# Optimization experiments

Hardware: AMD Instinct MI355X
Metric: run time of the kernel (lower is better)

Reference implementation:

```python
import jax, jax.numpy as jnp
import numpy as np

N_NODES = 50000
N_EDGES = 800000
N_FEAT = 128
HIDDEN = 16
N_CLASSES = 16


def spline_conv(x, src, dst, u, weight, root, bias, num_nodes):
    """SplineConv, dim=1, kernel_size=2, degree=1, open spline, aggr='mean'.

    x: [N, in], weight: [2, in, out], u: [E, 1] pseudo-coords in [0, 1).
    Linear B-spline basis over 2 knots: basis = (1-u, u) -> W[0], W[1].
    Transform at node level first (cheaper than per-edge when E > N),
    then gather along edges and scatter-mean to targets.
    """
    h = jnp.einsum('ni,kio->kno', x, weight)  # [2, N, out]
    msg = (1.0 - u) * h[0][src] + u * h[1][src]  # [E, out]
    agg = jax.ops.segment_sum(msg, dst, num_segments=num_nodes)
    deg = jax.ops.segment_sum(jnp.ones((src.shape[0],), x.dtype), dst,
                              num_segments=num_nodes)
    agg = agg / jnp.maximum(deg, 1.0)[:, None]
    return agg + x @ root + bias


def setup_inputs() -> dict:
    key = jax.random.key(0)
    ks = jax.random.split(key, 8)
    x = jax.random.normal(ks[0], (N_NODES, N_FEAT), dtype=jnp.float32)
    edge_index = jax.random.randint(ks[1], (2, N_EDGES), 0, N_NODES, dtype=jnp.int32)
    edge_attr = jax.random.uniform(ks[2], (N_EDGES, 1), dtype=jnp.float32)
    s1 = 1.0 / np.sqrt(N_FEAT)
    s2 = 1.0 / np.sqrt(HIDDEN)
    return {
        'x': x,
        'edge_index': edge_index,
        'edge_attr': edge_attr,
        'w1': jax.random.normal(ks[3], (2, N_FEAT, HIDDEN), dtype=jnp.float32) * s1,
        'root1': jax.random.normal(ks[4], (N_FEAT, HIDDEN), dtype=jnp.float32) * s1,
        'b1': jnp.zeros((HIDDEN,), dtype=jnp.float32),
        'w2': jax.random.normal(ks[5], (2, HIDDEN, N_CLASSES), dtype=jnp.float32) * s2,
        'root2': jax.random.normal(ks[6], (HIDDEN, N_CLASSES), dtype=jnp.float32) * s2,
        'b2': jnp.zeros((N_CLASSES,), dtype=jnp.float32),
    }


def reference(x, edge_index, edge_attr, w1, root1, b1, w2, root2, b2):
    src, dst = edge_index[0], edge_index[1]
    n = x.shape[0]
    # eval mode: F.dropout(training=False) is identity
    h = jax.nn.elu(spline_conv(x, src, dst, edge_attr, w1, root1, b1, n))
    out = spline_conv(h, src, dst, edge_attr, w2, root2, b2, n)
    return jax.nn.log_softmax(out, axis=1)
```

## Files before the change

### kernel.cpp

```cpp
#include <hip/hip_runtime.h>
#include <hip/hip_bf16.h>
#include <math.h>

#define N_NODES 50000
#define N_EDGES 800000
#define N_FEAT 128
#define HIDDEN 16
#define N_CLASSES 16

#define NBUCK 782
#define PB_NB 196
#define PB_E  4096
#define BCAP  1600

typedef __attribute__((ext_vector_type(8))) short short8v;
typedef __attribute__((ext_vector_type(4))) float floatx4;

__device__ __forceinline__ float bf2f(unsigned int bits16) {
    return __uint_as_float(bits16 << 16);
}
__device__ __forceinline__ unsigned int f2bf_bits(float f) {
    __hip_bfloat16 h = __float2bfloat16(f);
    return (unsigned int)*reinterpret_cast<unsigned short*>(&h);
}

__global__ __launch_bounds__(256) void k_node1(
    const float* __restrict__ x, const float* __restrict__ w1,
    const float* __restrict__ root1, const float* __restrict__ b1,
    unsigned int* __restrict__ ABu, float* __restrict__ C)
{
    int lane = threadIdx.x & 63;
    int wid  = threadIdx.x >> 6;
    int m = lane & 15;
    int q = lane >> 4;
    int nb = blockIdx.x * 64 + wid * 16;

    short8v bf[3][4];
#pragma unroll
    for (int c = 0; c < 4; ++c) {
        int k0 = c * 32 + q * 8;
        const float* p0 = w1 + (size_t)k0 * 16 + m;
        const float* p1 = w1 + 2048 + (size_t)k0 * 16 + m;
        const float* p2 = root1 + (size_t)k0 * 16 + m;
#pragma unroll
        for (int j = 0; j < 8; ++j) {
            bf[0][c][j] = (short)f2bf_bits(p0[j * 16]);
            bf[1][c][j] = (short)f2bf_bits(p1[j * 16]);
            bf[2][c][j] = (short)f2bf_bits(p2[j * 16]);
        }
    }

    int row = min(nb + m, N_NODES - 1);
    const float* xr = x + (size_t)row * N_FEAT;
    short8v af[4];
#pragma unroll
    for (int c = 0; c < 4; ++c) {
        int k0 = c * 32 + q * 8;
        float4 v0 = *(const float4*)(xr + k0);
        float4 v1 = *(const float4*)(xr + k0 + 4);
        af[c][0] = (short)f2bf_bits(v0.x); af[c][1] = (short)f2bf_bits(v0.y);
        af[c][2] = (short)f2bf_bits(v0.z); af[c][3] = (short)f2bf_bits(v0.w);
        af[c][4] = (short)f2bf_bits(v1.x); af[c][5] = (short)f2bf_bits(v1.y);
        af[c][6] = (short)f2bf_bits(v1.z); af[c][7] = (short)f2bf_bits(v1.w);
    }

    floatx4 acc0 = {0.f, 0.f, 0.f, 0.f};
    floatx4 acc1 = {0.f, 0.f, 0.f, 0.f};
    floatx4 acc2 = {0.f, 0.f, 0.f, 0.f};
#pragma unroll
    for (int c = 0; c < 4; ++c) {
        acc0 = __builtin_amdgcn_mfma_f32_16x16x32_bf16(af[c], bf[0][c], acc0, 0, 0, 0);
        acc1 = __builtin_amdgcn_mfma_f32_16x16x32_bf16(af[c], bf[1][c], acc1, 0, 0, 0);
        acc2 = __builtin_amdgcn_mfma_f32_16x16x32_bf16(af[c], bf[2][c], acc2, 0, 0, 0);
    }

    float bo = b1[m];
#pragma unroll
    for (int j = 0; j < 4; ++j) {
        int n = nb + q * 4 + j;
        if (n < N_NODES) {
            ABu[(size_t)n * 16 + m] = (f2bf_bits(acc1[j]) << 16) | f2bf_bits(acc0[j]);
            C[(size_t)n * 16 + m]   = acc2[j] + bo;
        }
    }
}

__global__ __launch_bounds__(256) void k_histA(
    const int* __restrict__ dst, int* __restrict__ blk)
{
    __shared__ int cnt[NBUCK];
    for (int i = threadIdx.x; i < NBUCK; i += 256) cnt[i] = 0;
    __syncthreads();
    int base = blockIdx.x * PB_E;
#pragma unroll
    for (int k = 0; k < PB_E / 256; ++k) {
        int e = base + k * 256 + threadIdx.x;
        if (e < N_EDGES) atomicAdd(&cnt[dst[e] >> 6], 1);
    }
    __syncthreads();
    for (int i = threadIdx.x; i < NBUCK; i += 256)
        blk[i * PB_NB + blockIdx.x] = cnt[i];
}

__global__ __launch_bounds__(256) void k_scanblk(
    int* __restrict__ blk, int* __restrict__ bucktot)
{
    __shared__ int s[256];
    int b = blockIdx.x, t = threadIdx.x;
    int v = (t < PB_NB) ? blk[b * PB_NB + t] : 0;
    s[t] = v;
    __syncthreads();
#pragma unroll
    for (int off = 1; off < 256; off <<= 1) {
        int w = (t >= off) ? s[t - off] : 0;
        __syncthreads();
        s[t] += w;
        __syncthreads();
    }
    if (t < PB_NB) blk[b * PB_NB + t] = s[t] - v;
    if (t == PB_NB - 1) bucktot[b] = s[t];
}

__global__ __launch_bounds__(1024) void k_scanbase(
    const int* __restrict__ bucktot, int* __restrict__ buckbase)
{
    __shared__ int s[1024];
    int t = threadIdx.x;
    int v = (t < NBUCK) ? bucktot[t] : 0;
    s[t] = v;
    __syncthreads();
#pragma unroll
    for (int off = 1; off < 1024; off <<= 1) {
        int w = (t >= off) ? s[t - off] : 0;
        __syncthreads();
        s[t] += w;
        __syncthreads();
    }
    if (t < NBUCK) buckbase[t] = s[t] - v;
    if (t == 0) buckbase[NBUCK] = N_EDGES;
}

__global__ __launch_bounds__(256) void k_partition(
    const int* __restrict__ src, const int* __restrict__ dst,
    const float* __restrict__ u, const int* __restrict__ buckbase,
    const int* __restrict__ blk, int2* __restrict__ epb)
{
    __shared__ int rank[NBUCK];
    __shared__ int base_s[NBUCK];
    for (int i = threadIdx.x; i < NBUCK; i += 256) {
        rank[i] = 0;
        base_s[i] = buckbase[i] + blk[i * PB_NB + blockIdx.x];
    }
    __syncthreads();
    int ebase = blockIdx.x * PB_E;
#pragma unroll
    for (int k = 0; k < PB_E / 256; ++k) {
        int e = ebase + k * 256 + threadIdx.x;
        if (e < N_EDGES) {
            int d = dst[e];
            int b = d >> 6;
            int pos = base_s[b] + atomicAdd(&rank[b], 1);
            epb[pos] = make_int2((src[e] & 0xFFFF) | ((d & 63) << 16),
                                 __float_as_int(u[e]));
        }
    }
}

__global__ __launch_bounds__(256) void k_bsort(
    const int* __restrict__ buckbase, int2* __restrict__ epb,
    int* __restrict__ rowptr)
{
    __shared__ int2 buf[BCAP];
    __shared__ int2 sorted[BCAP];
    __shared__ int cnt[64], cur[64];
    int b = blockIdx.x;
    int beg = buckbase[b], end = buckbase[b + 1];
    int m = min(end - beg, BCAP);

    if (threadIdx.x < 64) cnt[threadIdx.x] = 0;
    __syncthreads();
    for (int i = threadIdx.x; i < m; i += 256) {
        int2 p = epb[beg + i];
        buf[i] = p;
        atomicAdd(&cnt[(p.x >> 16) & 63], 1);
    }
    __syncthreads();
    if (threadIdx.x < 64) {
        int v = cnt[threadIdx.x];
        int s = v;
#pragma unroll
        for (int off = 1; off < 64; off <<= 1) {
            int w = __shfl_up(s, off);
            if (threadIdx.x >= off) s += w;
        }
        int ex = s - v;
        cur[threadIdx.x] = ex;
        int n = (b << 6) + threadIdx.x;
        if (n <= N_NODES) rowptr[n] = beg + ex;
    }
    __syncthreads();
    for (int i = threadIdx.x; i < m; i += 256) {
        int2 p = buf[i];
        int pos = atomicAdd(&cur[(p.x >> 16) & 63], 1);
        sorted[pos] = p;
    }
    __syncthreads();
    for (int i = threadIdx.x; i < m; i += 256)
        epb[beg + i] = sorted[i];
}

__global__ __launch_bounds__(256) void k_gather1(
    const int* __restrict__ rowptr, const int2* __restrict__ ep,
    const unsigned int* __restrict__ ABu, float* __restrict__ AGG)
{
    int n    = (blockIdx.x * 256 + threadIdx.x) >> 6;
    int lane = threadIdx.x & 63;
    int g = lane >> 3;
    int l = lane & 7;
    int beg = rowptr[n], end = rowptr[n + 1];
    const uint2* AB2 = (const uint2*)ABu;
    float ax = 0.f, ay = 0.f;
    int e = beg + g;
    for (; e + 8 < end; e += 16) {
        int2 p0 = ep[e];
        int2 p1 = ep[e + 8];
        float u0 = __int_as_float(p0.y);
        float u1 = __int_as_float(p1.y);
        uint2 q0 = AB2[(size_t)(p0.x & 0xFFFF) * 8 + l];
        uint2 q1 = AB2[(size_t)(p1.x & 0xFFFF) * 8 + l];
        ax += (1.f - u0) * bf2f(q0.x & 0xFFFF) + u0 * bf2f(q0.x >> 16);
        ay += (1.f - u0) * bf2f(q0.y & 0xFFFF) + u0 * bf2f(q0.y >> 16);
        ax += (1.f - u1) * bf2f(q1.x & 0xFFFF) + u1 * bf2f(q1.x >> 16);
        ay += (1.f - u1) * bf2f(q1.y & 0xFFFF) + u1 * bf2f(q1.y >> 16);
    }
    if (e < end) {
        int2 p0 = ep[e];
        float u0 = __int_as_float(p0.y);
        uint2 q0 = AB2[(size_t)(p0.x & 0xFFFF) * 8 + l];
        ax += (1.f - u0) * bf2f(q0.x & 0xFFFF) + u0 * bf2f(q0.x >> 16);
        ay += (1.f - u0) * bf2f(q0.y & 0xFFFF) + u0 * bf2f(q0.y >> 16);
    }
#pragma unroll
    for (int s = 8; s < 64; s <<= 1) {
        ax += __shfl_xor(ax, s);
        ay += __shfl_xor(ay, s);
    }
    float dv = fmaxf((float)(end - beg), 1.f);
    if (lane < 8)
        *(float2*)&AGG[(size_t)n * 16 + 2 * lane] = make_float2(ax / dv, ay / dv);
}

__global__ __launch_bounds__(256) void k_node2(
    const float* __restrict__ agg, float* __restrict__ C,
    const float* __restrict__ w2, const float* __restrict__ root2,
    const float* __restrict__ b2, unsigned int* __restrict__ ABu)
{
    __shared__ float W2[16 * 48];
    __shared__ float hl[16][17];
    for (int t = threadIdx.x; t < 16 * 48; t += 256) {
        int j = t / 48, o = t % 48;
        float v;
        if (o < 16)       v = w2[j * 16 + o];
        else if (o < 32)  v = w2[256 + j * 16 + (o - 16)];
        else              v = root2[j * 16 + (o - 32)];
        W2[t] = v;
    }
    int nl = threadIdx.x >> 4;
    int o  = threadIdx.x & 15;
    int n  = blockIdx.x * 16 + nl;

    float pre = agg[(size_t)n * 16 + o] + C[(size_t)n * 16 + o];
    float h   = pre > 0.f ? pre : expm1f(pre);
    __syncthreads();
    hl[nl][o] = h;
    __syncthreads();

    float a = 0.f, b = 0.f, p = 0.f;
#pragma unroll
    for (int j = 0; j < 16; ++j) {
        float hv = hl[nl][j];
        a += hv * W2[j * 48 + o];
        b += hv * W2[j * 48 + 16 + o];
        p += hv * W2[j * 48 + 32 + o];
    }
    ABu[(size_t)n * 16 + o] = (f2bf_bits(b) << 16) | f2bf_bits(a);
    C[(size_t)n * 16 + o] = p + b2[o];
}

__global__ __launch_bounds__(256) void k_gather2(
    const int* __restrict__ rowptr, const int2* __restrict__ ep,
    const unsigned int* __restrict__ ABu, const float* __restrict__ C,
    float* __restrict__ out)
{
    int n    = (blockIdx.x * 256 + threadIdx.x) >> 6;
    int lane = threadIdx.x & 63;
    int g = lane >> 3;
    int l = lane & 7;
    int beg = rowptr[n], end = rowptr[n + 1];
    const uint2* AB2 = (const uint2*)ABu;
    float ax = 0.f, ay = 0.f;
    int e = beg + g;
    for (; e + 8 < end; e += 16) {
        int2 p0 = ep[e];
        int2 p1 = ep[e + 8];
        float u0 = __int_as_float(p0.y);
        float u1 = __int_as_float(p1.y);
        uint2 q0 = AB2[(size_t)(p0.x & 0xFFFF) * 8 + l];
        uint2 q1 = AB2[(size_t)(p1.x & 0xFFFF) * 8 + l];
        ax += (1.f - u0) * bf2f(q0.x & 0xFFFF) + u0 * bf2f(q0.x >> 16);
        ay += (1.f - u0) * bf2f(q0.y & 0xFFFF) + u0 * bf2f(q0.y >> 16);
        ax += (1.f - u1) * bf2f(q1.x & 0xFFFF) + u1 * bf2f(q1.x >> 16);
        ay += (1.f - u1) * bf2f(q1.y & 0xFFFF) + u1 * bf2f(q1.y >> 16);
    }
    if (e < end) {
        int2 p0 = ep[e];
        float u0 = __int_as_float(p0.y);
        uint2 q0 = AB2[(size_t)(p0.x & 0xFFFF) * 8 + l];
        ax += (1.f - u0) * bf2f(q0.x & 0xFFFF) + u0 * bf2f(q0.x >> 16);
        ay += (1.f - u0) * bf2f(q0.y & 0xFFFF) + u0 * bf2f(q0.y >> 16);
    }
#pragma unroll
    for (int s = 8; s < 64; s <<= 1) {
        ax += __shfl_xor(ax, s);
        ay += __shfl_xor(ay, s);
    }
    float dv = fmaxf((float)(end - beg), 1.f);
    float2 cv = *(const float2*)&C[(size_t)n * 16 + 2 * l];
    float v0 = ax / dv + cv.x;
    float v1 = ay / dv + cv.y;

    float m = fmaxf(v0, v1);
#pragma unroll
    for (int s = 1; s < 8; s <<= 1) m = fmaxf(m, __shfl_xor(m, s));
    float ssum = __expf(v0 - m) + __expf(v1 - m);
#pragma unroll
    for (int s = 1; s < 8; s <<= 1) ssum += __shfl_xor(ssum, s);
    float lse = m + __logf(ssum);
    if (lane < 8)
        *(float2*)&out[(size_t)n * 16 + 2 * l] = make_float2(v0 - lse, v1 - lse);
}

extern "C" void kernel_launch(void* const* d_in, const int* in_sizes, int n_in,
                              void* d_out, int out_size, void* d_ws, size_t ws_size,
                              hipStream_t stream) {
    const float* x     = (const float*)d_in[0];
    const int*   ei    = (const int*)d_in[1];
    const float* ea    = (const float*)d_in[2];
    const float* w1    = (const float*)d_in[3];
    const float* root1 = (const float*)d_in[4];
    const float* b1    = (const float*)d_in[5];
    const float* w2    = (const float*)d_in[6];
    const float* root2 = (const float*)d_in[7];
    const float* b2    = (const float*)d_in[8];
    float* out = (float*)d_out;

    char* ws = (char*)d_ws;
    unsigned int* ABu = (unsigned int*)ws;
    float* C        = (float*)(ABu + (size_t)N_NODES * 16);
    float* AGG      = C + (size_t)N_NODES * 16;
    int2*  EPB      = (int2*)(AGG + (size_t)N_NODES * 16);
    int*   BLK      = (int*)(EPB + N_EDGES);
    int*   BUCKTOT  = BLK + NBUCK * PB_NB;
    int*   BUCKBASE = BUCKTOT + NBUCK;
    int*   ROWPTR   = BUCKBASE + (NBUCK + 1);

    const int* srcp = ei;
    const int* dstp = ei + N_EDGES;

    k_node1<<<782, 256, 0, stream>>>(x, w1, root1, b1, ABu, C);
    k_histA<<<PB_NB, 256, 0, stream>>>(dstp, BLK);
    k_scanblk<<<NBUCK, 256, 0, stream>>>(BLK, BUCKTOT);
    k_scanbase<<<1, 1024, 0, stream>>>(BUCKTOT, BUCKBASE);
    k_partition<<<PB_NB, 256, 0, stream>>>(srcp, dstp, ea, BUCKBASE, BLK, EPB);
    k_bsort<<<NBUCK, 256, 0, stream>>>(BUCKBASE, EPB, ROWPTR);

    k_gather1<<<N_NODES / 4, 256, 0, stream>>>(ROWPTR, EPB, ABu, AGG);
    k_node2<<<N_NODES / 16, 256, 0, stream>>>(AGG, C, w2, root2, b2, ABu);
    k_gather2<<<N_NODES / 4, 256, 0, stream>>>(ROWPTR, EPB, ABu, C, out);
}
```

Before: 96.93 us.

## Use fixed-capacity buckets to drop scans and fuse layer-2 node transform into gather

Replaces the histogram, two scan kernels and partition pass with one partition kernel. Each bucket now has a fixed slot of BCAP edges, and blocks reserve their range through a global atomic counter, so the prefix scans go away. Row begin and end arrays replace the contiguous rowptr. The layer-1 gather is fused with the ELU and the layer-2 node transform using wave shuffles, which removes the AGG round-trip and one kernel launch. The cost is nondeterministic edge order within a bucket, and any bucket holding more than BCAP edges is silently truncated.

```diff
diff --git a/kernel.cpp b/kernel.cpp
--- a/kernel.cpp
+++ b/kernel.cpp
@@ -85,97 +85,52 @@
     }
 }
 
-__global__ __launch_bounds__(256) void k_histA(
-    const int* __restrict__ dst, int* __restrict__ blk)
+__global__ __launch_bounds__(256) void k_part(
+    const int* __restrict__ src, const int* __restrict__ dst,
+    const float* __restrict__ u, int* __restrict__ rank,
+    int2* __restrict__ epb)
 {
     __shared__ int cnt[NBUCK];
     for (int i = threadIdx.x; i < NBUCK; i += 256) cnt[i] = 0;
     __syncthreads();
-    int base = blockIdx.x * PB_E;
-#pragma unroll
-    for (int k = 0; k < PB_E / 256; ++k) {
-        int e = base + k * 256 + threadIdx.x;
-        if (e < N_EDGES) atomicAdd(&cnt[dst[e] >> 6], 1);
-    }
-    __syncthreads();
-    for (int i = threadIdx.x; i < NBUCK; i += 256)
-        blk[i * PB_NB + blockIdx.x] = cnt[i];
-}
-
-__global__ __launch_bounds__(256) void k_scanblk(
-    int* __restrict__ blk, int* __restrict__ bucktot)
-{
-    __shared__ int s[256];
-    int b = blockIdx.x, t = threadIdx.x;
-    int v = (t < PB_NB) ? blk[b * PB_NB + t] : 0;
-    s[t] = v;
-    __syncthreads();
-#pragma unroll
-    for (int off = 1; off < 256; off <<= 1) {
-        int w = (t >= off) ? s[t - off] : 0;
-        __syncthreads();
-        s[t] += w;
-        __syncthreads();
-    }
-    if (t < PB_NB) blk[b * PB_NB + t] = s[t] - v;
-    if (t == PB_NB - 1) bucktot[b] = s[t];
-}
-
-__global__ __launch_bounds__(1024) void k_scanbase(
-    const int* __restrict__ bucktot, int* __restrict__ buckbase)
-{
-    __shared__ int s[1024];
-    int t = threadIdx.x;
-    int v = (t < NBUCK) ? bucktot[t] : 0;
-    s[t] = v;
-    __syncthreads();
-#pragma unroll
-    for (int off = 1; off < 1024; off <<= 1) {
-        int w = (t >= off) ? s[t - off] : 0;
-        __syncthreads();
-        s[t] += w;
-        __syncthreads();
-    }
-    if (t < NBUCK) buckbase[t] = s[t] - v;
-    if (t == 0) buckbase[NBUCK] = N_EDGES;
-}
-
-__global__ __launch_bounds__(256) void k_partition(
-    const int* __restrict__ src, const int* __restrict__ dst,
-    const float* __restrict__ u, const int* __restrict__ buckbase,
-    const int* __restrict__ blk, int2* __restrict__ epb)
-{
-    __shared__ int rank[NBUCK];
-    __shared__ int base_s[NBUCK];
-    for (int i = threadIdx.x; i < NBUCK; i += 256) {
-        rank[i] = 0;
-        base_s[i] = buckbase[i] + blk[i * PB_NB + blockIdx.x];
-    }
-    __syncthreads();
     int ebase = blockIdx.x * PB_E;
+    int myd[PB_E / 256];
 #pragma unroll
     for (int k = 0; k < PB_E / 256; ++k) {
         int e = ebase + k * 256 + threadIdx.x;
-        if (e < N_EDGES) {
-            int d = dst[e];
-            int b = d >> 6;
-            int pos = base_s[b] + atomicAdd(&rank[b], 1);
-            epb[pos] = make_int2((src[e] & 0xFFFF) | ((d & 63) << 16),
-                                 __float_as_int(u[e]));
+        myd[k] = (e < N_EDGES) ? dst[e] : -1;
+        if (myd[k] >= 0) atomicAdd(&cnt[myd[k] >> 6], 1);
+    }
+    __syncthreads();
+    for (int i = threadIdx.x; i < NBUCK; i += 256) {
+        int c = cnt[i];
+        int base = (c > 0) ? atomicAdd(&rank[i], c) : 0;
+        cnt[i] = i * BCAP + base;
+    }
+    __syncthreads();
+#pragma unroll
+    for (int k = 0; k < PB_E / 256; ++k) {
+        if (myd[k] >= 0) {
+            int e = ebase + k * 256 + threadIdx.x;
+            int b = myd[k] >> 6;
+            int pos = atomicAdd(&cnt[b], 1);
+            if (pos < (b + 1) * BCAP)
+                epb[pos] = make_int2((src[e] & 0xFFFF) | ((myd[k] & 63) << 16),
+                                     __float_as_int(u[e]));
         }
     }
 }
 
 __global__ __launch_bounds__(256) void k_bsort(
-    const int* __restrict__ buckbase, int2* __restrict__ epb,
-    int* __restrict__ rowptr)
+    const int* __restrict__ rank, int2* __restrict__ epb,
+    int* __restrict__ rowbeg, int* __restrict__ rowend)
 {
     __shared__ int2 buf[BCAP];
     __shared__ int2 sorted[BCAP];
     __shared__ int cnt[64], cur[64];
     int b = blockIdx.x;
-    int beg = buckbase[b], end = buckbase[b + 1];
-    int m = min(end - beg, BCAP);
+    int beg = b * BCAP;
+    int m = min(rank[b], BCAP);
 
     if (threadIdx.x < 64) cnt[threadIdx.x] = 0;
     __syncthreads();
@@ -196,7 +151,10 @@
         int ex = s - v;
         cur[threadIdx.x] = ex;
         int n = (b << 6) + threadIdx.x;
-        if (n <= N_NODES) rowptr[n] = beg + ex;
+        if (n < N_NODES) {
+            rowbeg[n] = beg + ex;
+            rowend[n] = beg + ex + v;
+        }
     }
     __syncthreads();
     for (int i = threadIdx.x; i < m; i += 256) {
@@ -209,15 +167,29 @@
         epb[beg + i] = sorted[i];
 }
 
-__global__ __launch_bounds__(256) void k_gather1(
-    const int* __restrict__ rowptr, const int2* __restrict__ ep,
-    const unsigned int* __restrict__ ABu, float* __restrict__ AGG)
-{
+__global__ __launch_bounds__(256) void k_gfused1(
+    const int* __restrict__ rowbeg, const int* __restrict__ rowend,
+    const int2* __restrict__ ep, const unsigned int* __restrict__ ABu,
+    const float* __restrict__ C, const float* __restrict__ w2,
+    const float* __restrict__ root2, const float* __restrict__ b2,
+    unsigned int* __restrict__ ABu2, float* __restrict__ C2)
+{
+    __shared__ float W2s[16 * 48];
+    for (int t = threadIdx.x; t < 16 * 48; t += 256) {
+        int j = t / 48, o = t % 48;
+        float v;
+        if (o < 16)       v = w2[j * 16 + o];
+        else if (o < 32)  v = w2[256 + j * 16 + (o - 16)];
+        else              v = root2[j * 16 + (o - 32)];
+        W2s[t] = v;
+    }
+    __syncthreads();
+
     int n    = (blockIdx.x * 256 + threadIdx.x) >> 6;
     int lane = threadIdx.x & 63;
     int g = lane >> 3;
     int l = lane & 7;
-    int beg = rowptr[n], end = rowptr[n + 1];
+    int beg = rowbeg[n], end = rowend[n];
     const uint2* AB2 = (const uint2*)ABu;
     float ax = 0.f, ay = 0.f;
     int e = beg + g;
@@ -246,57 +218,37 @@
         ay += __shfl_xor(ay, s);
     }
     float dv = fmaxf((float)(end - beg), 1.f);
-    if (lane < 8)
-        *(float2*)&AGG[(size_t)n * 16 + 2 * lane] = make_float2(ax / dv, ay / dv);
-}
-
-__global__ __launch_bounds__(256) void k_node2(
-    const float* __restrict__ agg, float* __restrict__ C,
-    const float* __restrict__ w2, const float* __restrict__ root2,
-    const float* __restrict__ b2, unsigned int* __restrict__ ABu)
-{
-    __shared__ float W2[16 * 48];
-    __shared__ float hl[16][17];
-    for (int t = threadIdx.x; t < 16 * 48; t += 256) {
-        int j = t / 48, o = t % 48;
-        float v;
-        if (o < 16)       v = w2[j * 16 + o];
-        else if (o < 32)  v = w2[256 + j * 16 + (o - 16)];
-        else              v = root2[j * 16 + (o - 32)];
-        W2[t] = v;
-    }
-    int nl = threadIdx.x >> 4;
-    int o  = threadIdx.x & 15;
-    int n  = blockIdx.x * 16 + nl;
-
-    float pre = agg[(size_t)n * 16 + o] + C[(size_t)n * 16 + o];
-    float h   = pre > 0.f ? pre : expm1f(pre);
-    __syncthreads();
-    hl[nl][o] = h;
-    __syncthreads();
-
-    float a = 0.f, b = 0.f, p = 0.f;
-#pragma unroll
-    for (int j = 0; j < 16; ++j) {
-        float hv = hl[nl][j];
-        a += hv * W2[j * 48 + o];
-        b += hv * W2[j * 48 + 16 + o];
-        p += hv * W2[j * 48 + 32 + o];
-    }
-    ABu[(size_t)n * 16 + o] = (f2bf_bits(b) << 16) | f2bf_bits(a);
-    C[(size_t)n * 16 + o] = p + b2[o];
+    float2 cv = *(const float2*)&C[(size_t)n * 16 + 2 * l];
+    float pre0 = ax / dv + cv.x;
+    float pre1 = ay / dv + cv.y;
+    float h0 = pre0 > 0.f ? pre0 : expm1f(pre0);
+    float h1 = pre1 > 0.f ? pre1 : expm1f(pre1);
+
+    int oc = (lane < 48) ? lane : 0;
+    float val = 0.f;
+#pragma unroll
+    for (int j2 = 0; j2 < 8; ++j2) {
+        float hh0 = __shfl(h0, j2);
+        float hh1 = __shfl(h1, j2);
+        val += hh0 * W2s[(2 * j2) * 48 + oc] + hh1 * W2s[(2 * j2 + 1) * 48 + oc];
+    }
+    float bval = __shfl(val, (lane + 16) & 63);
+    if (lane < 16)
+        ABu2[(size_t)n * 16 + lane] = (f2bf_bits(bval) << 16) | f2bf_bits(val);
+    else if (lane >= 32 && lane < 48)
+        C2[(size_t)n * 16 + (lane - 32)] = val + b2[lane - 32];
 }
 
 __global__ __launch_bounds__(256) void k_gather2(
-    const int* __restrict__ rowptr, const int2* __restrict__ ep,
-    const unsigned int* __restrict__ ABu, const float* __restrict__ C,
-    float* __restrict__ out)
+    const int* __restrict__ rowbeg, const int* __restrict__ rowend,
+    const int2* __restrict__ ep, const unsigned int* __restrict__ ABu,
+    const float* __restrict__ C, float* __restrict__ out)
 {
     int n    = (blockIdx.x * 256 + threadIdx.x) >> 6;
     int lane = threadIdx.x & 63;
     int g = lane >> 3;
     int l = lane & 7;
-    int beg = rowptr[n], end = rowptr[n + 1];
+    int beg = rowbeg[n], end = rowend[n];
     const uint2* AB2 = (const uint2*)ABu;
     float ax = 0.f, ay = 0.f;
     int e = beg + g;
@@ -355,26 +307,24 @@
     float* out = (float*)d_out;
 
     char* ws = (char*)d_ws;
-    unsigned int* ABu = (unsigned int*)ws;
-    float* C        = (float*)(ABu + (size_t)N_NODES * 16);
-    float* AGG      = C + (size_t)N_NODES * 16;
-    int2*  EPB      = (int2*)(AGG + (size_t)N_NODES * 16);
-    int*   BLK      = (int*)(EPB + N_EDGES);
-    int*   BUCKTOT  = BLK + NBUCK * PB_NB;
-    int*   BUCKBASE = BUCKTOT + NBUCK;
-    int*   ROWPTR   = BUCKBASE + (NBUCK + 1);
+    unsigned int* ABu  = (unsigned int*)ws;
+    unsigned int* ABu2 = ABu + (size_t)N_NODES * 16;
+    float* C    = (float*)(ABu2 + (size_t)N_NODES * 16);
+    float* C2   = C + (size_t)N_NODES * 16;
+    int2*  EPB  = (int2*)(C2 + (size_t)N_NODES * 16);
+    int* RANK   = (int*)(EPB + (size_t)NBUCK * BCAP);
+    int* ROWBEG = RANK + NBUCK;
+    int* ROWEND = ROWBEG + N_NODES;
 
     const int* srcp = ei;
     const int* dstp = ei + N_EDGES;
 
+    hipMemsetAsync(RANK, 0, NBUCK * sizeof(int), stream);
+
     k_node1<<<782, 256, 0, stream>>>(x, w1, root1, b1, ABu, C);
-    k_histA<<<PB_NB, 256, 0, stream>>>(dstp, BLK);
-    k_scanblk<<<NBUCK, 256, 0, stream>>>(BLK, BUCKTOT);
-    k_scanbase<<<1, 1024, 0, stream>>>(BUCKTOT, BUCKBASE);
-    k_partition<<<PB_NB, 256, 0, stream>>>(srcp, dstp, ea, BUCKBASE, BLK, EPB);
-    k_bsort<<<NBUCK, 256, 0, stream>>>(BUCKBASE, EPB, ROWPTR);
-
-    k_gather1<<<N_NODES / 4, 256, 0, stream>>>(ROWPTR, EPB, ABu, AGG);
-    k_node2<<<N_NODES / 16, 256, 0, stream>>>(AGG, C, w2, root2, b2, ABu);
-    k_gather2<<<N_NODES / 4, 256, 0, stream>>>(ROWPTR, EPB, ABu, C, out);
-}
+    k_part<<<PB_NB, 256, 0, stream>>>(srcp, dstp, ea, RANK, EPB);
+    k_bsort<<<NBUCK, 256, 0, stream>>>(RANK, EPB, ROWBEG, ROWEND);
+    k_gfused1<<<N_NODES / 4, 256, 0, stream>>>(ROWBEG, ROWEND, EPB, ABu, C,
+                                               w2, root2, b2, ABu2, C2);
+    k_gather2<<<N_NODES / 4, 256, 0, stream>>>(ROWBEG, ROWEND, EPB, ABu2, C2, out);
+}
```

Measured after the change: 96.46 us. Within noise of the previous version (-0.5%).
